# Performance work log

Measured on AMD Instinct MI355X. Metric: run time of the kernel, lower is better.

## Reference

```python
import jax, jax.numpy as jnp
import numpy as np

B, T, D, H = 4, 1024, 512, 8
DH = D // H
MLP = 4 * D
EPS = 1e-6


def _clinear(xr, xi, Wr, Wi, br, bi):
    # Naive complex Linear = two real nn.Linear layers (each adds its own bias):
    # re = Lr(xr) - Li(xi), im = Lr(xi) + Li(xr)
    re = xr @ Wr.T - xi @ Wi.T + (br - bi)
    im = xi @ Wr.T + xr @ Wi.T + (br + bi)
    return re, im


def _cln(xr, xi):
    # NaiveComplexLayerNorm: real LayerNorm (no affine) on re and im separately
    def ln(v):
        m = jnp.mean(v, -1, keepdims=True)
        va = jnp.var(v, -1, keepdims=True)
        return (v - m) * jax.lax.rsqrt(va + EPS)
    return ln(xr), ln(xi)


def _modulate(xr, xi, shr, shi, scr, sci):
    # complex x * (1 + scale) + shift, scale/shift are [B,D] broadcast over seq
    a, b = (1.0 + scr)[:, None, :], sci[:, None, :]
    return xr * a - xi * b + shr[:, None, :], xr * b + xi * a + shi[:, None, :]


def _gate(gr, gi, xr, xi):
    a, b = gr[:, None, :], gi[:, None, :]
    return xr * a - xi * b, xr * b + xi * a


def _heads(x):  # [B,T,D] -> [B,H,T,DH]
    return x.reshape(B, T, H, DH).transpose(0, 2, 1, 3)


def reference(x_re, x_im, c_re, c_im,
              ada_Wr, ada_Wi, ada_br, ada_bi,
              q_Wr, q_Wi, q_br, q_bi,
              k_Wr, k_Wi, k_br, k_bi,
              v_Wr, v_Wi, v_br, v_bi,
              o_Wr, o_Wi, o_br, o_bi,
              f1_Wr, f1_Wi, f1_br, f1_bi,
              f2_Wr, f2_Wi, f2_br, f2_bi):
    # adaLN_modulation: complex SiLU -> complex Linear -> 6 chunks along dim 1
    sr, si = jax.nn.silu(c_re), jax.nn.silu(c_im)
    mr, mi = _clinear(sr, si, ada_Wr, ada_Wi, ada_br, ada_bi)
    sh_ar, sc_ar, g_ar, sh_mr, sc_mr, g_mr = jnp.split(mr, 6, axis=1)
    sh_ai, sc_ai, g_ai, sh_mi, sc_mi, g_mi = jnp.split(mi, 6, axis=1)

    nr, ni = _cln(x_re, x_im)
    hr, hi = _modulate(nr, ni, sh_ar, sh_ai, sc_ar, sc_ai)

    qr, qi = _clinear(hr, hi, q_Wr, q_Wi, q_br, q_bi)
    kr, ki = _clinear(hr, hi, k_Wr, k_Wi, k_br, k_bi)
    vr, vi = _clinear(hr, hi, v_Wr, v_Wi, v_br, v_bi)
    qr, qi, kr, ki, vr, vi = map(_heads, (qr, qi, kr, ki, vr, vi))

    scale = 1.0 / jnp.sqrt(jnp.float32(DH))
    # complex scores q @ k^T (no conjugation, matching plain complex matmul)
    s_re = (jnp.einsum('bhqd,bhkd->bhqk', qr, kr) - jnp.einsum('bhqd,bhkd->bhqk', qi, ki)) * scale
    s_im = (jnp.einsum('bhqd,bhkd->bhqk', qr, ki) + jnp.einsum('bhqd,bhkd->bhqk', qi, kr)) * scale
    # naive complex softmax: real softmax applied to re/im independently
    a_re = jax.nn.softmax(s_re, axis=-1)
    a_im = jax.nn.softmax(s_im, axis=-1)
    o_r = jnp.einsum('bhqk,bhkd->bhqd', a_re, vr) - jnp.einsum('bhqk,bhkd->bhqd', a_im, vi)
    o_i = jnp.einsum('bhqk,bhkd->bhqd', a_re, vi) + jnp.einsum('bhqk,bhkd->bhqd', a_im, vr)
    o_r = o_r.transpose(0, 2, 1, 3).reshape(B, T, D)
    o_i = o_i.transpose(0, 2, 1, 3).reshape(B, T, D)
    o_r, o_i = _clinear(o_r, o_i, o_Wr, o_Wi, o_br, o_bi)

    gr, gi = _gate(g_ar, g_ai, o_r, o_i)
    x_re, x_im = x_re + gr, x_im + gi

    # ---- MLP branch
    nr, ni = _cln(x_re, x_im)
    hr, hi = _modulate(nr, ni, sh_mr, sh_mi, sc_mr, sc_mi)
    hr, hi = _clinear(hr, hi, f1_Wr, f1_Wi, f1_br, f1_bi)
    hr = jax.nn.gelu(hr, approximate=True)  # ComplexGELU(tanh) per component
    hi = jax.nn.gelu(hi, approximate=True)
    hr, hi = _clinear(hr, hi, f2_Wr, f2_Wi, f2_br, f2_bi)
    gr, gi = _gate(g_mr, g_mi, hr, hi)
    return jnp.stack([x_re + gr, x_im + gi])  # [2,B,T,D] = (real, imag)


def setup_inputs() -> dict:
    key = jax.random.key(0)
    ks = iter(jax.random.split(key, 48))

    def rn(shape, s=1.0):
        return jax.random.normal(next(ks), shape, dtype=jnp.float32) * s

    inp = {'x_re': rn((B, T, D)), 'x_im': rn((B, T, D)),
           'c_re': rn((B, D)), 'c_im': rn((B, D))}

    def lin(name, din, dout):
        inp[name + '_Wr'] = rn((dout, din), 0.02)
        inp[name + '_Wi'] = rn((dout, din), 0.02)
        inp[name + '_br'] = rn((dout,), 0.02)
        inp[name + '_bi'] = rn((dout,), 0.02)

    lin('ada', D, 6 * D)
    for n in ('q', 'k', 'v', 'o'):
        lin(n, D, D)
    lin('f1', D, MLP)
    lin('f2', MLP, D)
    return inp
```

## Files before the change

### kernel.cpp

```cpp
#include <hip/hip_runtime.h>


typedef unsigned short u16;
typedef unsigned int   u32;
typedef __attribute__((ext_vector_type(8))) __bf16 bf16x8;
typedef __attribute__((ext_vector_type(8))) u16    u16x8;
typedef __attribute__((ext_vector_type(4))) u16    u16x4;
typedef __attribute__((ext_vector_type(4))) float  f32x4;

#define MFMA16(a, b, c) __builtin_amdgcn_mfma_f32_16x16x32_bf16(a, b, c, 0, 0, 0)

static constexpr int Bd = 4, Td = 1024, Dd = 512, Hd = 8, DHd = 64, MLPd = 2048;
static constexpr size_t ACTe = (size_t)Bd * Td * Dd;

__device__ __forceinline__ u16 f2bf(float x) {
  unsigned int u = __builtin_bit_cast(unsigned int, x);
  u += 0x7fffu + ((u >> 16) & 1u);
  return (u16)(u >> 16);
}
__device__ __forceinline__ bf16x8 ldsfrag(const u16* p) {
  return __builtin_bit_cast(bf16x8, *(const u16x8*)p);
}
__device__ __forceinline__ bf16x8 negbf(bf16x8 v) {
  u16x8 u = __builtin_bit_cast(u16x8, v);
  u ^= (u16)0x8000;
  return __builtin_bit_cast(bf16x8, u);
}
__device__ __forceinline__ float gelu_tanh(float x) {
  float t = tanhf(0.7978845608028654f * (x + 0.044715f * x * x * x));
  return 0.5f * x * (1.f + t);
}
__device__ __forceinline__ void gload_lds16(const u16* g, u16* l) {
  __builtin_amdgcn_global_load_lds(
      (const __attribute__((address_space(1))) u32*)g,
      (__attribute__((address_space(3))) u32*)l, 16, 0, 0);
}

struct CJobs {
  const float* src[12];
  u16* dst[12];
  int blk_start[13];
};
__global__ __launch_bounds__(256) void convert_kernel(CJobs J) {
  const int blk = blockIdx.x;
  int jj = 0;
  while (jj < 11 && blk >= J.blk_start[jj + 1]) ++jj;
  const int idx = (blk - J.blk_start[jj]) * 256 + threadIdx.x;
  const float4 v = ((const float4*)J.src[jj])[idx];
  u16x4 o;
  o[0] = f2bf(v.x); o[1] = f2bf(v.y); o[2] = f2bf(v.z); o[3] = f2bf(v.w);
  *(u16x4*)(J.dst[jj] + (size_t)idx * 4) = o;
}

__global__ __launch_bounds__(256) void ada_kernel(
    const float* __restrict__ c_re, const float* __restrict__ c_im,
    const float* __restrict__ Wr, const float* __restrict__ Wi,
    const float* __restrict__ br, const float* __restrict__ bi,
    float* __restrict__ m_r, float* __restrict__ m_i) {
  __shared__ __align__(16) float sr[512], si[512];
  const int b = blockIdx.x / 12, nb = blockIdx.x % 12;
  const int tid = threadIdx.x;
  for (int i = tid; i < 512; i += 256) {
    const float xr = c_re[b * 512 + i], xi = c_im[b * 512 + i];
    sr[i] = xr / (1.f + __expf(-xr));
    si[i] = xi / (1.f + __expf(-xi));
  }
  __syncthreads();
  const int n = nb * 256 + tid;
  const float4* wr4 = (const float4*)(Wr + (size_t)n * 512);
  const float4* wi4 = (const float4*)(Wi + (size_t)n * 512);
  const float4* sr4 = (const float4*)sr;
  const float4* si4 = (const float4*)si;
  float ar = 0.f, ai = 0.f;
  for (int k = 0; k < 128; ++k) {
    const float4 a_ = sr4[k], b_ = si4[k], u = wr4[k], v = wi4[k];
    ar += a_.x * u.x - b_.x * v.x + a_.y * u.y - b_.y * v.y +
          a_.z * u.z - b_.z * v.z + a_.w * u.w - b_.w * v.w;
    ai += b_.x * u.x + a_.x * v.x + b_.y * u.y + a_.y * v.y +
          b_.z * u.z + a_.z * v.z + b_.w * u.w + a_.w * v.w;
  }
  m_r[(size_t)b * 3072 + n] = ar + br[n] - bi[n];
  m_i[(size_t)b * 3072 + n] = ai + br[n] + bi[n];
}

__global__ __launch_bounds__(256) void ln_mod_kernel(
    const float* __restrict__ xr, const float* __restrict__ xi,
    const float* __restrict__ mv_r, const float* __restrict__ mv_i,
    int off_sh, int off_sc,
    u16* __restrict__ hr, u16* __restrict__ hi) {
  const int row = blockIdx.x;
  const int b = row >> 10;
  const int tid = threadIdx.x;
  const float* xrp = xr + (size_t)row * 512;
  const float* xip = xi + (size_t)row * 512;
  const float r0 = xrp[tid], r1 = xrp[tid + 256];
  const float i0 = xip[tid], i1 = xip[tid + 256];
  float s0 = r0 + r1, s1 = r0 * r0 + r1 * r1;
  float s2 = i0 + i1, s3 = i0 * i0 + i1 * i1;
  #pragma unroll
  for (int o = 32; o > 0; o >>= 1) {
    s0 += __shfl_down(s0, o); s1 += __shfl_down(s1, o);
    s2 += __shfl_down(s2, o); s3 += __shfl_down(s3, o);
  }
  __shared__ float red[4][4];
  if ((tid & 63) == 0) {
    const int wv = tid >> 6;
    red[wv][0] = s0; red[wv][1] = s1; red[wv][2] = s2; red[wv][3] = s3;
  }
  __syncthreads();
  s0 = red[0][0] + red[1][0] + red[2][0] + red[3][0];
  s1 = red[0][1] + red[1][1] + red[2][1] + red[3][1];
  s2 = red[0][2] + red[1][2] + red[2][2] + red[3][2];
  s3 = red[0][3] + red[1][3] + red[2][3] + red[3][3];
  const float mr = s0 * (1.f / 512.f), mi = s2 * (1.f / 512.f);
  const float vr = s1 * (1.f / 512.f) - mr * mr;
  const float vi = s3 * (1.f / 512.f) - mi * mi;
  const float rr = rsqrtf(vr + 1e-6f), ri = rsqrtf(vi + 1e-6f);
  const float* shr = mv_r + (size_t)b * 3072 + off_sh;
  const float* shi = mv_i + (size_t)b * 3072 + off_sh;
  const float* scr = mv_r + (size_t)b * 3072 + off_sc;
  const float* sci = mv_i + (size_t)b * 3072 + off_sc;
  #pragma unroll
  for (int jj = 0; jj < 2; ++jj) {
    const int n = tid + jj * 256;
    const float nr = ((jj ? r1 : r0) - mr) * rr;
    const float ni = ((jj ? i1 : i0) - mi) * ri;
    const float a = 1.f + scr[n], bb = sci[n];
    hr[(size_t)row * 512 + n] = f2bf(nr * a - ni * bb + shr[n]);
    hi[(size_t)row * 512 + n] = f2bf(nr * bb + ni * a + shi[n]);
  }
}

template <int NT, int EPI>
__global__ __launch_bounds__(NT, 6) void cgemm_kernel(
    const u16* __restrict__ Ar, const u16* __restrict__ Ai,
    const u16* __restrict__ W0r, const u16* __restrict__ W0i,
    const float* __restrict__ b0r, const float* __restrict__ b0i,
    const u16* __restrict__ W1r, const u16* __restrict__ W1i,
    const float* __restrict__ b1r, const float* __restrict__ b1i,
    const u16* __restrict__ W2r, const u16* __restrict__ W2i,
    const float* __restrict__ b2r, const float* __restrict__ b2i,
    int Klen, int ldk, int ntiles_per_seg, int out_ld,
    u16* __restrict__ o0r, u16* __restrict__ o0i,
    u16* __restrict__ o1r, u16* __restrict__ o1i,
    u16* __restrict__ o2r, u16* __restrict__ o2i,
    const float* __restrict__ resid_r, const float* __restrict__ resid_i,
    const float* __restrict__ gate_r, const float* __restrict__ gate_i,
    float* __restrict__ ofr, float* __restrict__ ofi) {
  constexpr int TM = (NT == 512) ? 128 : 64;
  constexpr int TN = 64;
  constexpr int NW = NT / 64;
  constexpr int ABLK = TM / 16, BBLK = TN / 16;
  constexpr int NSTAGE = 2 * (ABLK + BBLK);
  const int seg = blockIdx.y / ntiles_per_seg;
  const int n0 = (blockIdx.y % ntiles_per_seg) * TN;
  const int m0 = blockIdx.x * TM;
  const int kz = (EPI == 4) ? blockIdx.z : 0;
  const int kbase = kz * Klen;
  const u16* Wr = (seg == 0) ? W0r : (seg == 1) ? W1r : W2r;
  const u16* Wi = (seg == 0) ? W0i : (seg == 1) ? W1i : W2i;
  const float* br = (seg == 0) ? b0r : (seg == 1) ? b1r : b2r;
  const float* bi = (seg == 0) ? b0i : (seg == 1) ? b1i : b2i;
  u16* obr = (seg == 0) ? o0r : (seg == 1) ? o1r : o2r;
  u16* obi = (seg == 0) ? o0i : (seg == 1) ? o1i : o2i;

  __shared__ __align__(16) u16 sAr[TM * 32], sAi[TM * 32];
  __shared__ __align__(16) u16 sBr[TN * 32], sBi[TN * 32];

  const int tid = threadIdx.x;
  const int w = tid >> 6, lane = tid & 63;
  const int wm = w >> 1, wn = w & 1;
  const int q4 = lane >> 4, c = lane & 15;
  const int r16 = lane & 15, kc8 = (lane >> 4) * 8;

  const f32x4 z = {0.f, 0.f, 0.f, 0.f};
  f32x4 accR[2][2], accI[2][2];
  #pragma unroll
  for (int a = 0; a < 2; ++a)
    #pragma unroll
    for (int b2 = 0; b2 < 2; ++b2) { accR[a][b2] = z; accI[a][b2] = z; }

  for (int kt = 0; kt < Klen; kt += 32) {
    #pragma unroll
    for (int j = 0; j < NSTAGE / NW; ++j) {
      const int I = w + NW * j;
      const u16* src;
      u16* dst;
      if (I < ABLK) {
        src = Ar + (size_t)(m0 + I * 16 + r16) * ldk + kbase + kt + kc8;
        dst = sAr + I * 512;
      } else if (I < 2 * ABLK) {
        const int s = I - ABLK;
        src = Ai + (size_t)(m0 + s * 16 + r16) * ldk + kbase + kt + kc8;
        dst = sAi + s * 512;
      } else if (I < 2 * ABLK + BBLK) {
        const int s = I - 2 * ABLK;
        src = Wr + (size_t)(n0 + s * 16 + r16) * ldk + kbase + kt + kc8;
        dst = sBr + s * 512;
      } else {
        const int s = I - 2 * ABLK - BBLK;
        src = Wi + (size_t)(n0 + s * 16 + r16) * ldk + kbase + kt + kc8;
        dst = sBi + s * 512;
      }
      gload_lds16(src, dst);
    }
    asm volatile("s_waitcnt vmcnt(0)" ::: "memory");
    __syncthreads();
    bf16x8 a_r[2], a_i[2];
    #pragma unroll
    for (int mi = 0; mi < 2; ++mi) {
      a_r[mi] = ldsfrag(sAr + (wm * 2 + mi) * 512 + lane * 8);
      a_i[mi] = ldsfrag(sAi + (wm * 2 + mi) * 512 + lane * 8);
    }
    #pragma unroll
    for (int ni = 0; ni < 2; ++ni) {
      const bf16x8 b_r = ldsfrag(sBr + (wn * 2 + ni) * 512 + lane * 8);
      const bf16x8 b_i = ldsfrag(sBi + (wn * 2 + ni) * 512 + lane * 8);
      const bf16x8 b_n = negbf(b_i);
      #pragma unroll
      for (int mi = 0; mi < 2; ++mi) {
        accR[mi][ni] = MFMA16(a_r[mi], b_r, accR[mi][ni]);
        accR[mi][ni] = MFMA16(a_i[mi], b_n, accR[mi][ni]);
        accI[mi][ni] = MFMA16(a_i[mi], b_r, accI[mi][ni]);
        accI[mi][ni] = MFMA16(a_r[mi], b_i, accI[mi][ni]);
      }
    }
    __syncthreads();
  }

  const float scale = (EPI == 0 && seg == 0) ? 0.125f : 1.f;
  #pragma unroll
  for (int mi = 0; mi < 2; ++mi)
    #pragma unroll
    for (int ni = 0; ni < 2; ++ni) {
      const int n = n0 + wn * 32 + ni * 16 + c;
      const float biasr = (EPI == 4) ? 0.f : br[n] - bi[n];
      const float biasi = (EPI == 4) ? 0.f : br[n] + bi[n];
      #pragma unroll
      for (int r = 0; r < 4; ++r) {
        const int m = m0 + wm * 32 + mi * 16 + q4 * 4 + r;
        const float ore = accR[mi][ni][r] + biasr;
        const float oim = accI[mi][ni][r] + biasi;
        if (EPI == 0) {
          obr[(size_t)m * out_ld + n] = f2bf(ore * scale);
          obi[(size_t)m * out_ld + n] = f2bf(oim * scale);
        } else if (EPI == 2) {
          obr[(size_t)m * out_ld + n] = f2bf(gelu_tanh(ore));
          obi[(size_t)m * out_ld + n] = f2bf(gelu_tanh(oim));
        } else if (EPI == 4) {
          const size_t o = (size_t)kz * 4096 * out_ld + (size_t)m * out_ld + n;
          ofr[o] = ore;
          ofi[o] = oim;
        } else {
          const int bb = m >> 10;
          const float gr = gate_r[(size_t)bb * 3072 + n];
          const float gi = gate_i[(size_t)bb * 3072 + n];
          const size_t o = (size_t)m * 512 + n;
          ofr[o] = resid_r[o] + ore * gr - oim * gi;
          ofi[o] = resid_i[o] + ore * gi + oim * gr;
        }
      }
    }
}

__global__ __launch_bounds__(256) void f2fuse_kernel(
    const float* __restrict__ p_r, const float* __restrict__ p_i,
    const float* __restrict__ br, const float* __restrict__ bi,
    const float* __restrict__ gate_r, const float* __restrict__ gate_i,
    const float* __restrict__ x2r, const float* __restrict__ x2i,
    float* __restrict__ outr, float* __restrict__ outi) {
  const size_t e = ((size_t)blockIdx.x * 256 + threadIdx.x) * 4;
  const int n = (int)(e & 511);
  const int m = (int)(e >> 9);
  const int b = m >> 10;
  const float4 a0 = *(const float4*)(p_r + e);
  const float4 a1 = *(const float4*)(p_r + ACTe + e);
  const float4 c0 = *(const float4*)(p_i + e);
  const float4 c1 = *(const float4*)(p_i + ACTe + e);
  const float4 vbr = *(const float4*)(br + n);
  const float4 vbi = *(const float4*)(bi + n);
  const float4 vgr = *(const float4*)(gate_r + (size_t)b * 3072 + n);
  const float4 vgi = *(const float4*)(gate_i + (size_t)b * 3072 + n);
  const float4 xr = *(const float4*)(x2r + e);
  const float4 xi = *(const float4*)(x2i + e);
  float4 orr, oii;
  {
    const float pr[4] = {a0.x + a1.x, a0.y + a1.y, a0.z + a1.z, a0.w + a1.w};
    const float pi[4] = {c0.x + c1.x, c0.y + c1.y, c0.z + c1.z, c0.w + c1.w};
    const float brr[4] = {vbr.x, vbr.y, vbr.z, vbr.w};
    const float bii[4] = {vbi.x, vbi.y, vbi.z, vbi.w};
    const float gr[4] = {vgr.x, vgr.y, vgr.z, vgr.w};
    const float gi[4] = {vgi.x, vgi.y, vgi.z, vgi.w};
    const float xrr[4] = {xr.x, xr.y, xr.z, xr.w};
    const float xii[4] = {xi.x, xi.y, xi.z, xi.w};
    float outr4[4], outi4[4];
    #pragma unroll
    for (int j = 0; j < 4; ++j) {
      const float ore = pr[j] + brr[j] - bii[j];
      const float oim = pi[j] + brr[j] + bii[j];
      outr4[j] = xrr[j] + ore * gr[j] - oim * gi[j];
      outi4[j] = xii[j] + ore * gi[j] + oim * gr[j];
    }
    orr = {outr4[0], outr4[1], outr4[2], outr4[3]};
    oii = {outi4[0], outi4[1], outi4[2], outi4[3]};
  }
  *(float4*)(outr + e) = orr;
  *(float4*)(outi + e) = oii;
}

__global__ __launch_bounds__(256) void vt_kernel(
    const u16* __restrict__ Vr, const u16* __restrict__ Vi,
    u16* __restrict__ vTr, u16* __restrict__ vTi) {
  __shared__ __align__(16) u16 tile[2][64 * 64];
  const int tid = threadIdx.x;
  const int tt = blockIdx.x, bh = blockIdx.y, b = bh >> 3, h = bh & 7;
  const size_t base = (size_t)b * Td * Dd + h * DHd;
  for (int idx = tid; idx < 512; idx += 256) {
    const int t = idx >> 3, dblk = idx & 7;
    const size_t g = base + (size_t)(tt * 64 + t) * Dd + dblk * 8;
    const int o = t * 64 + ((dblk ^ (t >> 3)) << 3);
    *(u16x8*)&tile[0][o] = *(const u16x8*)(Vr + g);
    *(u16x8*)&tile[1][o] = *(const u16x8*)(Vi + g);
  }
  __syncthreads();
  for (int idx = tid; idx < 512; idx += 256) {
    const int d = idx >> 3, cg = idx & 7;
    u16x8 o0, o1;
    #pragma unroll
    for (int j = 0; j < 8; ++j) {
      const int t = cg * 8 + j;
      const int o = t * 64 + (((d >> 3) ^ (t >> 3)) << 3) + (d & 7);
      o0[j] = tile[0][o];
      o1[j] = tile[1][o];
    }
    const size_t g = ((size_t)bh * 64 + d) * Td + tt * 64 + cg * 8;
    *(u16x8*)(vTr + g) = o0;
    *(u16x8*)(vTi + g) = o1;
  }
}

__global__ __launch_bounds__(256) void attn_kernel(
    const u16* __restrict__ Qr, const u16* __restrict__ Qi,
    const u16* __restrict__ Kr, const u16* __restrict__ Ki,
    const u16* __restrict__ vTr, const u16* __restrict__ vTi,
    u16* __restrict__ Or, u16* __restrict__ Oi) {
  __shared__ __align__(16) u16 sQV[2][64 * 72];
  __shared__ __align__(16) u16 sK[2][64 * 72];

  const int tid = threadIdx.x;
  const int w = tid >> 6, lane = tid & 63;
  const int q4 = lane >> 4, c = lane & 15;
  const int bh = blockIdx.y, b = bh >> 3, h = bh & 7;
  const int t0 = blockIdx.x * 64;
  const size_t base = (size_t)b * Td * Dd + h * DHd;
  const size_t vbase = (size_t)bh * 64 * Td;

  for (int idx = tid; idx < 512; idx += 256) {
    const int row = idx >> 3, cg = idx & 7;
    const size_t g = base + (size_t)(t0 + row) * Dd + cg * 8;
    const int lo = row * 72 + cg * 8;
    *(u16x8*)&sQV[0][lo] = *(const u16x8*)(Qr + g);
    *(u16x8*)&sQV[1][lo] = *(const u16x8*)(Qi + g);
  }
  __syncthreads();
  bf16x8 aQr[2], aQi[2], aQn[2];
  #pragma unroll
  for (int kc = 0; kc < 2; ++kc) {
    const int off = (w * 16 + c) * 72 + kc * 32 + q4 * 8;
    aQr[kc] = ldsfrag(&sQV[0][off]);
    aQi[kc] = ldsfrag(&sQV[1][off]);
    aQn[kc] = negbf(aQi[kc]);
  }
  __syncthreads();

  float mst[2][4], lst[2][4];
  #pragma unroll
  for (int p = 0; p < 2; ++p)
    for (int r = 0; r < 4; ++r) { mst[p][r] = -1e30f; lst[p][r] = 0.f; }
  const f32x4 z = {0.f, 0.f, 0.f, 0.f};
  f32x4 U1[4], U2[4], U3[4], U4[4];
  for (int i = 0; i < 4; ++i) { U1[i] = z; U2[i] = z; U3[i] = z; U4[i] = z; }

  for (int kt = 0; kt < 16; ++kt) {
    for (int idx = tid; idx < 512; idx += 256) {
      const int row = idx >> 3, cg = idx & 7;
      const int lo = row * 72 + cg * 8;
      const size_t gk = base + (size_t)(kt * 64 + row) * Dd + cg * 8;
      *(u16x8*)&sK[0][lo] = *(const u16x8*)(Kr + gk);
      *(u16x8*)&sK[1][lo] = *(const u16x8*)(Ki + gk);
      const size_t gv = vbase + (size_t)row * Td + kt * 64 + cg * 8;
      *(u16x8*)&sQV[0][lo] = *(const u16x8*)(vTr + gv);
      *(u16x8*)&sQV[1][lo] = *(const u16x8*)(vTi + gv);
    }
    __syncthreads();

    f32x4 S[2][4];
    #pragma unroll
    for (int nb = 0; nb < 4; ++nb) {
      f32x4 tr = z, ti = z;
      #pragma unroll
      for (int kc = 0; kc < 2; ++kc) {
        const int off = (nb * 16 + c) * 72 + kc * 32 + q4 * 8;
        const bf16x8 bKr = ldsfrag(&sK[0][off]);
        const bf16x8 bKi = ldsfrag(&sK[1][off]);
        tr = MFMA16(aQr[kc], bKr, tr);
        tr = MFMA16(aQn[kc], bKi, tr);
        ti = MFMA16(aQi[kc], bKr, ti);
        ti = MFMA16(aQr[kc], bKi, ti);
      }
      S[0][nb] = tr; S[1][nb] = ti;
    }
    __syncthreads();

    float alpha[2][4];
    #pragma unroll
    for (int p = 0; p < 2; ++p) {
      float rs[4];
      #pragma unroll
      for (int r = 0; r < 4; ++r) {
        float tm = fmaxf(fmaxf(S[p][0][r], S[p][1][r]), fmaxf(S[p][2][r], S[p][3][r]));
        #pragma unroll
        for (int o = 1; o < 16; o <<= 1) tm = fmaxf(tm, __shfl_xor(tm, o));
        const float mn = fmaxf(mst[p][r], tm);
        alpha[p][r] = __expf(mst[p][r] - mn);
        mst[p][r] = mn;
        rs[r] = 0.f;
      }
      #pragma unroll
      for (int nb = 0; nb < 4; ++nb)
        #pragma unroll
        for (int r = 0; r < 4; ++r) {
          const float pv = __expf(S[p][nb][r] - mst[p][r]);
          rs[r] += pv;
          sK[p][(w * 16 + q4 * 4 + r) * 72 + nb * 16 + c] = f2bf(pv);
        }
      #pragma unroll
      for (int r = 0; r < 4; ++r) {
        float s = rs[r];
        #pragma unroll
        for (int o = 1; o < 16; o <<= 1) s += __shfl_xor(s, o);
        lst[p][r] = lst[p][r] * alpha[p][r] + s;
      }
    }
    #pragma unroll
    for (int i = 0; i < 4; ++i)
      #pragma unroll
      for (int r = 0; r < 4; ++r) {
        U1[i][r] *= alpha[0][r]; U2[i][r] *= alpha[0][r];
        U3[i][r] *= alpha[1][r]; U4[i][r] *= alpha[1][r];
      }
    asm volatile("s_waitcnt lgkmcnt(0)" ::: "memory");
    #pragma unroll
    for (int kc = 0; kc < 2; ++kc) {
      const int poff = (w * 16 + c) * 72 + kc * 32 + q4 * 8;
      const bf16x8 aPr = ldsfrag(&sK[0][poff]);
      const bf16x8 aPi = ldsfrag(&sK[1][poff]);
      #pragma unroll
      for (int nd = 0; nd < 4; ++nd) {
        const int voff = (nd * 16 + c) * 72 + kc * 32 + q4 * 8;
        const bf16x8 bVr = ldsfrag(&sQV[0][voff]);
        const bf16x8 bVi = ldsfrag(&sQV[1][voff]);
        U1[nd] = MFMA16(aPr, bVr, U1[nd]);
        U2[nd] = MFMA16(aPr, bVi, U2[nd]);
        U3[nd] = MFMA16(aPi, bVr, U3[nd]);
        U4[nd] = MFMA16(aPi, bVi, U4[nd]);
      }
    }
    __syncthreads();
  }

  #pragma unroll
  for (int nd = 0; nd < 4; ++nd)
    #pragma unroll
    for (int r = 0; r < 4; ++r) {
      const int trow = t0 + w * 16 + q4 * 4 + r;
      const int d = nd * 16 + c;
      const float ilre = 1.f / lst[0][r], ilim = 1.f / lst[1][r];
      const float ore = U1[nd][r] * ilre - U4[nd][r] * ilim;
      const float oim = U2[nd][r] * ilre + U3[nd][r] * ilim;
      const size_t g = base + (size_t)trow * Dd + d;
      Or[g] = f2bf(ore);
      Oi[g] = f2bf(oim);
    }
}

extern "C" void kernel_launch(void* const* d_in, const int* in_sizes, int n_in,
                              void* d_out, int out_size, void* d_ws, size_t ws_size,
                              hipStream_t stream) {
  const float* x_re  = (const float*)d_in[0];
  const float* x_im  = (const float*)d_in[1];
  const float* c_re  = (const float*)d_in[2];
  const float* c_im  = (const float*)d_in[3];
  const float* adaWr = (const float*)d_in[4];
  const float* adaWi = (const float*)d_in[5];
  const float* adabr = (const float*)d_in[6];
  const float* adabi = (const float*)d_in[7];
  const float* qWr = (const float*)d_in[8],  *qWi = (const float*)d_in[9];
  const float* qbr = (const float*)d_in[10], *qbi = (const float*)d_in[11];
  const float* kWr = (const float*)d_in[12], *kWi = (const float*)d_in[13];
  const float* kbr = (const float*)d_in[14], *kbi = (const float*)d_in[15];
  const float* vWr = (const float*)d_in[16], *vWi = (const float*)d_in[17];
  const float* vbr = (const float*)d_in[18], *vbi = (const float*)d_in[19];
  const float* oWr = (const float*)d_in[20], *oWi = (const float*)d_in[21];
  const float* obr = (const float*)d_in[22], *obi = (const float*)d_in[23];
  const float* f1Wr = (const float*)d_in[24], *f1Wi = (const float*)d_in[25];
  const float* f1br = (const float*)d_in[26], *f1bi = (const float*)d_in[27];
  const float* f2Wr = (const float*)d_in[28], *f2Wi = (const float*)d_in[29];
  const float* f2br = (const float*)d_in[30], *f2bi = (const float*)d_in[31];

  char* wsp = (char*)d_ws;
  size_t off = 0;
  auto alloc = [&](size_t bytes) -> void* {
    void* p = wsp + off;
    off += (bytes + 255) & ~(size_t)255;
    return p;
  };
  const size_t WQ = 512 * 512, WF = 2048 * 512;
  u16* wqr = (u16*)alloc(WQ * 2); u16* wqi = (u16*)alloc(WQ * 2);
  u16* wkr = (u16*)alloc(WQ * 2); u16* wki = (u16*)alloc(WQ * 2);
  u16* wvr = (u16*)alloc(WQ * 2); u16* wvi = (u16*)alloc(WQ * 2);
  u16* wor = (u16*)alloc(WQ * 2); u16* woi = (u16*)alloc(WQ * 2);
  u16* wf1r = (u16*)alloc(WF * 2); u16* wf1i = (u16*)alloc(WF * 2);
  u16* wf2r = (u16*)alloc(WF * 2); u16* wf2i = (u16*)alloc(WF * 2);
  float* m_r = (float*)alloc(4 * 3072 * 4);
  float* m_i = (float*)alloc(4 * 3072 * 4);
  const size_t ACT = ACTe;
  u16* h1r = (u16*)alloc(ACT * 2); u16* h1i = (u16*)alloc(ACT * 2);
  u16* qbr_ = (u16*)alloc(ACT * 2); u16* qbi_ = (u16*)alloc(ACT * 2);
  u16* kbr_ = (u16*)alloc(ACT * 2); u16* kbi_ = (u16*)alloc(ACT * 2);
  u16* vbr_ = (u16*)alloc(ACT * 2); u16* vbi_ = (u16*)alloc(ACT * 2);
  u16* atr = (u16*)alloc(ACT * 2); u16* ati = (u16*)alloc(ACT * 2);
  float* x2r = (float*)alloc(ACT * 4); float* x2i = (float*)alloc(ACT * 4);
  u16* vtr = (u16*)alloc(ACT * 2); u16* vti = (u16*)alloc(ACT * 2);
  float* p_r = (float*)alloc(2 * ACT * 4);
  float* p_i = (float*)alloc(2 * ACT * 4);
  u16* h2r = h1r; u16* h2i = h1i;
  u16* f1or = qbr_;
  u16* f1oi = qbr_ + (size_t)Bd * Td * MLPd;

  CJobs J;
  const float* wsrc[12] = {qWr, qWi, kWr, kWi, vWr, vWi, oWr, oWi, f1Wr, f1Wi, f2Wr, f2Wi};
  u16* wdst[12] = {wqr, wqi, wkr, wki, wvr, wvi, wor, woi, wf1r, wf1i, wf2r, wf2i};
  int cum = 0;
  for (int j = 0; j < 12; ++j) {
    J.src[j] = wsrc[j]; J.dst[j] = wdst[j]; J.blk_start[j] = cum;
    cum += (j < 8 ? (int)WQ : (int)WF) / 1024;
  }
  J.blk_start[12] = cum;
  convert_kernel<<<cum, 256, 0, stream>>>(J);

  ada_kernel<<<48, 256, 0, stream>>>(c_re, c_im, adaWr, adaWi, adabr, adabi, m_r, m_i);

  ln_mod_kernel<<<4096, 256, 0, stream>>>(x_re, x_im, m_r, m_i, 0, 512, h1r, h1i);

  cgemm_kernel<512, 0><<<dim3(32, 24), 512, 0, stream>>>(
      h1r, h1i, wqr, wqi, qbr, qbi, wkr, wki, kbr, kbi, wvr, wvi, vbr, vbi,
      512, 512, 8, 512, qbr_, qbi_, kbr_, kbi_, vbr_, vbi_,
      nullptr, nullptr, nullptr, nullptr, nullptr, nullptr);

  vt_kernel<<<dim3(16, 32), 256, 0, stream>>>(vbr_, vbi_, vtr, vti);

  attn_kernel<<<dim3(16, 32), 256, 0, stream>>>(qbr_, qbi_, kbr_, kbi_, vtr, vti, atr, ati);

  cgemm_kernel<256, 1><<<dim3(64, 8), 256, 0, stream>>>(
      atr, ati, wor, woi, obr, obi, wor, woi, obr, obi, wor, woi, obr, obi,
      512, 512, 8, 512, nullptr, nullptr, nullptr, nullptr, nullptr, nullptr,
      x_re, x_im, m_r + 1024, m_i + 1024, x2r, x2i);

  ln_mod_kernel<<<4096, 256, 0, stream>>>(x2r, x2i, m_r, m_i, 1536, 2048, h2r, h2i);

  cgemm_kernel<512, 2><<<dim3(32, 32), 512, 0, stream>>>(
      h2r, h2i, wf1r, wf1i, f1br, f1bi, wf1r, wf1i, f1br, f1bi, wf1r, wf1i, f1br, f1bi,
      512, 512, 32, 2048, f1or, f1oi, nullptr, nullptr, nullptr, nullptr,
      nullptr, nullptr, nullptr, nullptr, nullptr, nullptr);

  cgemm_kernel<256, 4><<<dim3(64, 8, 2), 256, 0, stream>>>(
      f1or, f1oi, wf2r, wf2i, f2br, f2bi, wf2r, wf2i, f2br, f2bi, wf2r, wf2i, f2br, f2bi,
      1024, 2048, 8, 512, nullptr, nullptr, nullptr, nullptr, nullptr, nullptr,
      nullptr, nullptr, nullptr, nullptr, p_r, p_i);

  float* outp = (float*)d_out;
  f2fuse_kernel<<<(int)(ACT / 4 / 256), 256, 0, stream>>>(
      p_r, p_i, f2br, f2bi, m_r + 2560, m_i + 2560, x2r, x2i, outp, outp + ACT);
}
```

Baseline: 502.5 us.

## Split attention KV sequence across two wave groups and deepen GEMM K-step

```diff
diff --git a/kernel.cpp b/kernel.cpp
--- a/kernel.cpp
+++ b/kernel.cpp
@@ -151,7 +151,7 @@
   constexpr int TN = 64;
   constexpr int NW = NT / 64;
   constexpr int ABLK = TM / 16, BBLK = TN / 16;
-  constexpr int NSTAGE = 2 * (ABLK + BBLK);
+  constexpr int NCH = 4 * (ABLK + BBLK);
   const int seg = blockIdx.y / ntiles_per_seg;
   const int n0 = (blockIdx.y % ntiles_per_seg) * TN;
   const int m0 = blockIdx.x * TM;
@@ -164,8 +164,8 @@
   u16* obr = (seg == 0) ? o0r : (seg == 1) ? o1r : o2r;
   u16* obi = (seg == 0) ? o0i : (seg == 1) ? o1i : o2i;
 
-  __shared__ __align__(16) u16 sAr[TM * 32], sAi[TM * 32];
-  __shared__ __align__(16) u16 sBr[TN * 32], sBi[TN * 32];
+  __shared__ __align__(16) u16 sAr[TM * 64], sAi[TM * 64];
+  __shared__ __align__(16) u16 sBr[TN * 64], sBi[TN * 64];
 
   const int tid = threadIdx.x;
   const int w = tid >> 6, lane = tid & 63;
@@ -180,49 +180,55 @@
     #pragma unroll
     for (int b2 = 0; b2 < 2; ++b2) { accR[a][b2] = z; accI[a][b2] = z; }
 
-  for (int kt = 0; kt < Klen; kt += 32) {
-    #pragma unroll
-    for (int j = 0; j < NSTAGE / NW; ++j) {
+  for (int kt = 0; kt < Klen; kt += 64) {
+    #pragma unroll
+    for (int j = 0; j < NCH / NW; ++j) {
       const int I = w + NW * j;
       const u16* src;
       u16* dst;
-      if (I < ABLK) {
-        src = Ar + (size_t)(m0 + I * 16 + r16) * ldk + kbase + kt + kc8;
+      if (I < 2 * ABLK) {
+        const int b = I >> 1, sub = I & 1;
+        src = Ar + (size_t)(m0 + b * 16 + r16) * ldk + kbase + kt + sub * 32 + kc8;
         dst = sAr + I * 512;
-      } else if (I < 2 * ABLK) {
-        const int s = I - ABLK;
-        src = Ai + (size_t)(m0 + s * 16 + r16) * ldk + kbase + kt + kc8;
-        dst = sAi + s * 512;
-      } else if (I < 2 * ABLK + BBLK) {
-        const int s = I - 2 * ABLK;
-        src = Wr + (size_t)(n0 + s * 16 + r16) * ldk + kbase + kt + kc8;
-        dst = sBr + s * 512;
+      } else if (I < 4 * ABLK) {
+        const int I2 = I - 2 * ABLK, b = I2 >> 1, sub = I2 & 1;
+        src = Ai + (size_t)(m0 + b * 16 + r16) * ldk + kbase + kt + sub * 32 + kc8;
+        dst = sAi + I2 * 512;
+      } else if (I < 4 * ABLK + 2 * BBLK) {
+        const int I2 = I - 4 * ABLK, b = I2 >> 1, sub = I2 & 1;
+        src = Wr + (size_t)(n0 + b * 16 + r16) * ldk + kbase + kt + sub * 32 + kc8;
+        dst = sBr + I2 * 512;
       } else {
-        const int s = I - 2 * ABLK - BBLK;
-        src = Wi + (size_t)(n0 + s * 16 + r16) * ldk + kbase + kt + kc8;
-        dst = sBi + s * 512;
+        const int I2 = I - 4 * ABLK - 2 * BBLK, b = I2 >> 1, sub = I2 & 1;
+        src = Wi + (size_t)(n0 + b * 16 + r16) * ldk + kbase + kt + sub * 32 + kc8;
+        dst = sBi + I2 * 512;
       }
       gload_lds16(src, dst);
     }
     asm volatile("s_waitcnt vmcnt(0)" ::: "memory");
     __syncthreads();
-    bf16x8 a_r[2], a_i[2];
-    #pragma unroll
-    for (int mi = 0; mi < 2; ++mi) {
-      a_r[mi] = ldsfrag(sAr + (wm * 2 + mi) * 512 + lane * 8);
-      a_i[mi] = ldsfrag(sAi + (wm * 2 + mi) * 512 + lane * 8);
-    }
-    #pragma unroll
-    for (int ni = 0; ni < 2; ++ni) {
-      const bf16x8 b_r = ldsfrag(sBr + (wn * 2 + ni) * 512 + lane * 8);
-      const bf16x8 b_i = ldsfrag(sBi + (wn * 2 + ni) * 512 + lane * 8);
-      const bf16x8 b_n = negbf(b_i);
+    #pragma unroll
+    for (int sub = 0; sub < 2; ++sub) {
+      bf16x8 a_r[2], a_i[2];
       #pragma unroll
       for (int mi = 0; mi < 2; ++mi) {
-        accR[mi][ni] = MFMA16(a_r[mi], b_r, accR[mi][ni]);
-        accR[mi][ni] = MFMA16(a_i[mi], b_n, accR[mi][ni]);
-        accI[mi][ni] = MFMA16(a_i[mi], b_r, accI[mi][ni]);
-        accI[mi][ni] = MFMA16(a_r[mi], b_i, accI[mi][ni]);
+        const int blk = (wm * 2 + mi) * 2 + sub;
+        a_r[mi] = ldsfrag(sAr + blk * 512 + lane * 8);
+        a_i[mi] = ldsfrag(sAi + blk * 512 + lane * 8);
+      }
+      #pragma unroll
+      for (int ni = 0; ni < 2; ++ni) {
+        const int blk = (wn * 2 + ni) * 2 + sub;
+        const bf16x8 b_r = ldsfrag(sBr + blk * 512 + lane * 8);
+        const bf16x8 b_i = ldsfrag(sBi + blk * 512 + lane * 8);
+        const bf16x8 b_n = negbf(b_i);
+        #pragma unroll
+        for (int mi = 0; mi < 2; ++mi) {
+          accR[mi][ni] = MFMA16(a_r[mi], b_r, accR[mi][ni]);
+          accR[mi][ni] = MFMA16(a_i[mi], b_n, accR[mi][ni]);
+          accI[mi][ni] = MFMA16(a_i[mi], b_r, accI[mi][ni]);
+          accI[mi][ni] = MFMA16(a_r[mi], b_i, accI[mi][ni]);
+        }
       }
     }
     __syncthreads();
@@ -339,36 +345,38 @@
   }
 }
 
-__global__ __launch_bounds__(256) void attn_kernel(
+__global__ __launch_bounds__(512, 4) void attn_kernel(
     const u16* __restrict__ Qr, const u16* __restrict__ Qi,
     const u16* __restrict__ Kr, const u16* __restrict__ Ki,
     const u16* __restrict__ vTr, const u16* __restrict__ vTi,
     u16* __restrict__ Or, u16* __restrict__ Oi) {
-  __shared__ __align__(16) u16 sQV[2][64 * 72];
-  __shared__ __align__(16) u16 sK[2][64 * 72];
+  __shared__ __align__(16) u16 smem[36864];
+  u16* sK = smem;
+  u16* sV = smem + 18432;
 
   const int tid = threadIdx.x;
   const int w = tid >> 6, lane = tid & 63;
+  const int g = w >> 2, wl = w & 3;
   const int q4 = lane >> 4, c = lane & 15;
   const int bh = blockIdx.y, b = bh >> 3, h = bh & 7;
   const int t0 = blockIdx.x * 64;
   const size_t base = (size_t)b * Td * Dd + h * DHd;
   const size_t vbase = (size_t)bh * 64 * Td;
 
-  for (int idx = tid; idx < 512; idx += 256) {
-    const int row = idx >> 3, cg = idx & 7;
-    const size_t g = base + (size_t)(t0 + row) * Dd + cg * 8;
-    const int lo = row * 72 + cg * 8;
-    *(u16x8*)&sQV[0][lo] = *(const u16x8*)(Qr + g);
-    *(u16x8*)&sQV[1][lo] = *(const u16x8*)(Qi + g);
+  for (int idx = tid; idx < 1024; idx += 512) {
+    const int p = idx >> 9, pos = idx & 511;
+    const int row = pos >> 3, cg = pos & 7;
+    const size_t gq = base + (size_t)(t0 + row) * Dd + cg * 8;
+    *(u16x8*)&sV[p * 4608 + row * 72 + cg * 8] =
+        *(const u16x8*)((p ? Qi : Qr) + gq);
   }
   __syncthreads();
   bf16x8 aQr[2], aQi[2], aQn[2];
   #pragma unroll
   for (int kc = 0; kc < 2; ++kc) {
-    const int off = (w * 16 + c) * 72 + kc * 32 + q4 * 8;
-    aQr[kc] = ldsfrag(&sQV[0][off]);
-    aQi[kc] = ldsfrag(&sQV[1][off]);
+    const int off = (wl * 16 + c) * 72 + kc * 32 + q4 * 8;
+    aQr[kc] = ldsfrag(&sV[0 * 4608 + off]);
+    aQi[kc] = ldsfrag(&sV[1 * 4608 + off]);
     aQn[kc] = negbf(aQi[kc]);
   }
   __syncthreads();
@@ -381,16 +389,22 @@
   f32x4 U1[4], U2[4], U3[4], U4[4];
   for (int i = 0; i < 4; ++i) { U1[i] = z; U2[i] = z; U3[i] = z; U4[i] = z; }
 
-  for (int kt = 0; kt < 16; ++kt) {
-    for (int idx = tid; idx < 512; idx += 256) {
-      const int row = idx >> 3, cg = idx & 7;
+  for (int it = 0; it < 8; ++it) {
+    for (int idx = tid; idx < 4096; idx += 512) {
+      const int g2 = idx >> 11, rem = idx & 2047;
+      const int ps = rem >> 9, pos = rem & 511;
+      const int row = pos >> 3, cg = pos & 7;
+      const int kt = g2 * 8 + it;
       const int lo = row * 72 + cg * 8;
-      const size_t gk = base + (size_t)(kt * 64 + row) * Dd + cg * 8;
-      *(u16x8*)&sK[0][lo] = *(const u16x8*)(Kr + gk);
-      *(u16x8*)&sK[1][lo] = *(const u16x8*)(Ki + gk);
-      const size_t gv = vbase + (size_t)row * Td + kt * 64 + cg * 8;
-      *(u16x8*)&sQV[0][lo] = *(const u16x8*)(vTr + gv);
-      *(u16x8*)&sQV[1][lo] = *(const u16x8*)(vTi + gv);
+      if (ps < 2) {
+        const size_t gk = base + (size_t)(kt * 64 + row) * Dd + cg * 8;
+        *(u16x8*)&sK[(g2 * 2 + ps) * 4608 + lo] =
+            *(const u16x8*)((ps ? Ki : Kr) + gk);
+      } else {
+        const size_t gv = vbase + (size_t)row * Td + kt * 64 + cg * 8;
+        *(u16x8*)&sV[(g2 * 2 + (ps - 2)) * 4608 + lo] =
+            *(const u16x8*)(((ps - 2) ? vTi : vTr) + gv);
+      }
     }
     __syncthreads();
 
@@ -401,8 +415,8 @@
       #pragma unroll
       for (int kc = 0; kc < 2; ++kc) {
         const int off = (nb * 16 + c) * 72 + kc * 32 + q4 * 8;
-        const bf16x8 bKr = ldsfrag(&sK[0][off]);
-        const bf16x8 bKi = ldsfrag(&sK[1][off]);
+        const bf16x8 bKr = ldsfrag(&sK[(g * 2 + 0) * 4608 + off]);
+        const bf16x8 bKi = ldsfrag(&sK[(g * 2 + 1) * 4608 + off]);
         tr = MFMA16(aQr[kc], bKr, tr);
         tr = MFMA16(aQn[kc], bKi, tr);
         ti = MFMA16(aQi[kc], bKr, ti);
@@ -432,7 +446,7 @@
         for (int r = 0; r < 4; ++r) {
           const float pv = __expf(S[p][nb][r] - mst[p][r]);
           rs[r] += pv;
-          sK[p][(w * 16 + q4 * 4 + r) * 72 + nb * 16 + c] = f2bf(pv);
+          sK[(g * 2 + p) * 4608 + (wl * 16 + q4 * 4 + r) * 68 + nb * 16 + c] = f2bf(pv);
         }
       #pragma unroll
       for (int r = 0; r < 4; ++r) {
@@ -452,14 +466,14 @@
     asm volatile("s_waitcnt lgkmcnt(0)" ::: "memory");
     #pragma unroll
     for (int kc = 0; kc < 2; ++kc) {
-      const int poff = (w * 16 + c) * 72 + kc * 32 + q4 * 8;
-      const bf16x8 aPr = ldsfrag(&sK[0][poff]);
-      const bf16x8 aPi = ldsfrag(&sK[1][poff]);
+      const int poff = (wl * 16 + c) * 68 + kc * 32 + q4 * 8;
+      const bf16x8 aPr = ldsfrag(&sK[(g * 2 + 0) * 4608 + poff]);
+      const bf16x8 aPi = ldsfrag(&sK[(g * 2 + 1) * 4608 + poff]);
       #pragma unroll
       for (int nd = 0; nd < 4; ++nd) {
         const int voff = (nd * 16 + c) * 72 + kc * 32 + q4 * 8;
-        const bf16x8 bVr = ldsfrag(&sQV[0][voff]);
-        const bf16x8 bVi = ldsfrag(&sQV[1][voff]);
+        const bf16x8 bVr = ldsfrag(&sV[(g * 2 + 0) * 4608 + voff]);
+        const bf16x8 bVi = ldsfrag(&sV[(g * 2 + 1) * 4608 + voff]);
         U1[nd] = MFMA16(aPr, bVr, U1[nd]);
         U2[nd] = MFMA16(aPr, bVi, U2[nd]);
         U3[nd] = MFMA16(aPi, bVr, U3[nd]);
@@ -469,19 +483,67 @@
     __syncthreads();
   }
 
-  #pragma unroll
-  for (int nd = 0; nd < 4; ++nd)
-    #pragma unroll
-    for (int r = 0; r < 4; ++r) {
-      const int trow = t0 + w * 16 + q4 * 4 + r;
-      const int d = nd * 16 + c;
-      const float ilre = 1.f / lst[0][r], ilim = 1.f / lst[1][r];
-      const float ore = U1[nd][r] * ilre - U4[nd][r] * ilim;
-      const float oim = U2[nd][r] * ilre + U3[nd][r] * ilim;
-      const size_t g = base + (size_t)trow * Dd + d;
-      Or[g] = f2bf(ore);
-      Oi[g] = f2bf(oim);
-    }
+  float* fbuf = (float*)smem;
+  if (g == 1) {
+    #pragma unroll
+    for (int a = 0; a < 4; ++a) {
+      const f32x4* Us = (a == 0) ? U1 : (a == 1) ? U2 : (a == 2) ? U3 : U4;
+      #pragma unroll
+      for (int nd = 0; nd < 4; ++nd)
+        *(f32x4*)(fbuf + wl * 4096 + (a * 4 + nd) * 256 + lane * 4) = Us[nd];
+    }
+    if (c == 0) {
+      #pragma unroll
+      for (int p = 0; p < 2; ++p)
+        #pragma unroll
+        for (int r = 0; r < 4; ++r) {
+          const int row = wl * 16 + q4 * 4 + r;
+          fbuf[16384 + p * 64 + row] = mst[p][r];
+          fbuf[16640 + p * 64 + row] = lst[p][r];
+        }
+    }
+  }
+  __syncthreads();
+  if (g == 0) {
+    float a0[2][4], a1[2][4], lm[2][4];
+    #pragma unroll
+    for (int p = 0; p < 2; ++p)
+      #pragma unroll
+      for (int r = 0; r < 4; ++r) {
+        const int row = wl * 16 + q4 * 4 + r;
+        const float m1 = fbuf[16384 + p * 64 + row];
+        const float l1 = fbuf[16640 + p * 64 + row];
+        const float mn = fmaxf(mst[p][r], m1);
+        a0[p][r] = __expf(mst[p][r] - mn);
+        a1[p][r] = __expf(m1 - mn);
+        lm[p][r] = lst[p][r] * a0[p][r] + l1 * a1[p][r];
+      }
+    #pragma unroll
+    for (int a = 0; a < 4; ++a) {
+      f32x4* Us = (a == 0) ? U1 : (a == 1) ? U2 : (a == 2) ? U3 : U4;
+      const int p = (a >= 2) ? 1 : 0;
+      #pragma unroll
+      for (int nd = 0; nd < 4; ++nd) {
+        const f32x4 Up = *(const f32x4*)(fbuf + wl * 4096 + (a * 4 + nd) * 256 + lane * 4);
+        #pragma unroll
+        for (int r = 0; r < 4; ++r)
+          Us[nd][r] = Us[nd][r] * a0[p][r] + Up[r] * a1[p][r];
+      }
+    }
+    #pragma unroll
+    for (int nd = 0; nd < 4; ++nd)
+      #pragma unroll
+      for (int r = 0; r < 4; ++r) {
+        const int trow = t0 + wl * 16 + q4 * 4 + r;
+        const int d = nd * 16 + c;
+        const float ilre = 1.f / lm[0][r], ilim = 1.f / lm[1][r];
+        const float ore = U1[nd][r] * ilre - U4[nd][r] * ilim;
+        const float oim = U2[nd][r] * ilre + U3[nd][r] * ilim;
+        const size_t gg = base + (size_t)trow * Dd + d;
+        Or[gg] = f2bf(ore);
+        Oi[gg] = f2bf(oim);
+      }
+  }
 }
 
 extern "C" void kernel_launch(void* const* d_in, const int* in_sizes, int n_in,
@@ -560,7 +622,7 @@
 
   vt_kernel<<<dim3(16, 32), 256, 0, stream>>>(vbr_, vbi_, vtr, vti);
 
-  attn_kernel<<<dim3(16, 32), 256, 0, stream>>>(qbr_, qbi_, kbr_, kbi_, vtr, vti, atr, ati);
+  attn_kernel<<<dim3(16, 32), 512, 0, stream>>>(qbr_, qbi_, kbr_, kbi_, vtr, vti, atr, ati);
 
   cgemm_kernel<256, 1><<<dim3(64, 8), 256, 0, stream>>>(
       atr, ati, wor, woi, obr, obi, wor, woi, obr, obi, wor, woi, obr, obi,
```

After: 632.4 us. 1.26x slower.
